# Kernel tuning notes

Hardware: AMD Instinct MI355X
Metric: run time of the kernel (lower is better)

Reference implementation:

```python
import jax, jax.numpy as jnp
import numpy as np

E = 1152          # embed_dim (Qwen3-VL vision hidden_size)
H = 16            # num_heads
D = E // H        # head_dim = 72
SEG = 8           # number of frames / attention segments
HW = 32           # each frame is 32x32 patches -> seg_len = 1024
L = HW * HW
S = SEG * L       # total tokens = 8192


def _make_rotary(S):
    # VisionRotaryEmbedding(dim=head_dim//2): inv_freq over arange(0, 36, 2)/36 -> 18 freqs
    half = D // 2  # 36
    inv_freq = 1.0 / (10000.0 ** (jnp.arange(0, half, 2, dtype=jnp.float32) / half))  # (18,)
    # 2D (h,w) position ids within each 32x32 frame, tiled across frames
    hpos = jnp.tile(jnp.repeat(jnp.arange(HW, dtype=jnp.float32), HW), SEG)  # (S,)
    wpos = jnp.tile(jnp.tile(jnp.arange(HW, dtype=jnp.float32), HW), SEG)    # (S,)
    fh = hpos[:, None] * inv_freq[None, :]   # (S, 18)
    fw = wpos[:, None] * inv_freq[None, :]   # (S, 18)
    freqs = jnp.concatenate([fh, fw], axis=-1)       # (S, 36)
    emb = jnp.concatenate([freqs, freqs], axis=-1)   # (S, 72) = head_dim
    return jnp.cos(emb), jnp.sin(emb)


def setup_inputs() -> dict:
    key = jax.random.key(0)
    k = jax.random.split(key, 6)
    std = 1.0 / np.sqrt(E)
    cos, sin = _make_rotary(S)
    return {
        "x": jax.random.normal(k[0], (S, E), jnp.float32),
        "cos": cos,
        "sin": sin,
        "qkv_w": jax.random.normal(k[1], (3 * E, E), jnp.float32) * std,
        "qkv_b": jax.random.normal(k[2], (3 * E,), jnp.float32) * 0.02,
        "proj_w": jax.random.normal(k[3], (E, E), jnp.float32) * std,
        "proj_b": jax.random.normal(k[4], (E,), jnp.float32) * 0.02,
        "cu_seqlens": jnp.arange(SEG + 1, dtype=jnp.int32) * L,
    }


def _rope(t, cos, sin):
    # t: (S, H, D); cos/sin: (S, D) broadcast over heads (matches cos.unsqueeze(1))
    half = t.shape[-1] // 2
    t1, t2 = t[..., :half], t[..., half:]
    rot = jnp.concatenate([-t2, t1], axis=-1)
    return t * cos[:, None, :] + rot * sin[:, None, :]


def reference(x, cos, sin, qkv_w, qkv_b, proj_w, proj_b, cu_seqlens):
    S_, E_ = x.shape
    qkv = x @ qkv_w.T + qkv_b                     # (S, 3E)
    q, k, v = jnp.split(qkv, 3, axis=-1)
    q = _rope(q.reshape(S_, H, D), cos, sin)
    k = _rope(k.reshape(S_, H, D), cos, sin)
    v = v.reshape(S_, H, D)
    # Equal-length segments (one per frame): block-diagonal attention via reshape,
    # honoring cu_seqlens structure without materializing an (S, S) mask.
    nseg = cu_seqlens.shape[0] - 1
    Lseg = S_ // nseg
    qs = q.reshape(nseg, Lseg, H, D)
    ks = k.reshape(nseg, Lseg, H, D)
    vs = v.reshape(nseg, Lseg, H, D)
    scale = 1.0 / np.sqrt(D)
    logits = jnp.einsum('gqhd,gkhd->ghqk', qs, ks) * scale   # (nseg, H, L, L)
    attn = jax.nn.softmax(logits, axis=-1)
    out = jnp.einsum('ghqk,gkhd->gqhd', attn, vs).reshape(S_, E_)
    return out @ proj_w.T + proj_b
```

## Files before the change

### kernel.cpp

```cpp
#include <hip/hip_runtime.h>
#include <hip/hip_bf16.h>
#include <stdint.h>

#define SEGN 8
#define LSEG 1024
#define SS   8192
#define EE   1152
#define HH   16
#define DD   72
#define DP   96
#define E3   3456
#define E3P  3584

typedef __attribute__((ext_vector_type(8))) __bf16 bf16x8;
typedef __attribute__((ext_vector_type(4))) float  f32x4;

__device__ __forceinline__ short f2b(float x) {
  __hip_bfloat16 h = __float2bfloat16(x);
  return __builtin_bit_cast(short, h);
}
__device__ __forceinline__ float b2f(short x) {
  return __bfloat162float(__builtin_bit_cast(__hip_bfloat16, x));
}
__device__ __forceinline__ void gload16(const void* g, void* l) {
  __builtin_amdgcn_global_load_lds(
      (const __attribute__((address_space(1))) unsigned int*)g,
      (__attribute__((address_space(3))) unsigned int*)l, 16, 0, 0);
}

#define BAR() __builtin_amdgcn_s_barrier()
#define LGKM0() do { asm volatile("s_waitcnt lgkmcnt(0)" ::: "memory"); \
                     __builtin_amdgcn_sched_barrier(0); } while (0)

__global__ void k_cvt(const float* __restrict__ in, short* __restrict__ out, int n4) {
  int i = blockIdx.x * blockDim.x + threadIdx.x;
  int stride = gridDim.x * blockDim.x;
  for (; i < n4; i += stride) {
    float4 v = reinterpret_cast<const float4*>(in)[i];
    short4 o;
    o.x = f2b(v.x); o.y = f2b(v.y); o.z = f2b(v.z); o.w = f2b(v.w);
    reinterpret_cast<short4*>(out)[i] = o;
  }
}

__global__ __launch_bounds__(512, 2) void k_gemm256(
    const short* __restrict__ A, const short* __restrict__ B,
    const float* __restrict__ bias, short* __restrict__ C,
    int M, int K, int Nreal)
{
  __shared__ __align__(16) short As[3][256 * 32];
  __shared__ __align__(16) short Bs[3][256 * 32];
  const int t = threadIdx.x;
  const int lane = t & 63, wave = t >> 6;
  const int r16 = lane & 15, kg = lane >> 4;
  const int wm = wave >> 2, wn = wave & 3;
  const int m0 = blockIdx.x * 256, n0 = blockIdx.y * 256;
  const int NT = K >> 5;

  const int D0 = t * 16, D1 = (t + 512) * 16;
  const int L0 = D0 ^ (((D0 >> 7) & 3) << 4);
  const int L1 = D1 ^ (((D1 >> 7) & 3) << 4);
  const int sr0 = L0 >> 6, sc0 = (L0 & 63) >> 1;
  const int sr1 = L1 >> 6, sc1 = (L1 & 63) >> 1;
  const short* pA0 = A + (size_t)(m0 + sr0) * K + sc0;
  const short* pA1 = A + (size_t)(m0 + sr1) * K + sc1;
  const short* pB0 = B + (size_t)(n0 + sr0) * K + sc0;
  const short* pB1 = B + (size_t)(n0 + sr1) * K + sc1;

  const int xorv = ((r16 >> 1) & 3) << 4;
  const int abase = (wm * 128 + r16) * 64 + ((kg * 16) ^ xorv);
  const int bbase = (wn * 64 + r16) * 64 + ((kg * 16) ^ xorv);

  f32x4 acc[8][4] = {};

  gload16(pA0, (char*)As[0] + D0); gload16(pA1, (char*)As[0] + D1);
  gload16(pB0, (char*)Bs[0] + D0); gload16(pB1, (char*)Bs[0] + D1);
  gload16(pA0 + 32, (char*)As[1] + D0); gload16(pA1 + 32, (char*)As[1] + D1);
  gload16(pB0 + 32, (char*)Bs[1] + D0); gload16(pB1 + 32, (char*)Bs[1] + D1);
  asm volatile("s_waitcnt vmcnt(4)" ::: "memory");
  BAR();

  int cur = 0;
  for (int kt = 0; kt < NT; ++kt) {
    int nb = cur + 2; if (nb >= 3) nb -= 3;
    const char* bufA = (const char*)As[cur];
    const char* bufB = (const char*)Bs[cur];
    const bool pf = (kt + 2 < NT);
    const int koff = (kt + 2) * 32;

    bf16x8 a_[4], b_[4];
#pragma unroll
    for (int m = 0; m < 4; ++m)
      a_[m] = *(const bf16x8*)(bufA + abase + m * 1024);
#pragma unroll
    for (int n = 0; n < 4; ++n)
      b_[n] = *(const bf16x8*)(bufB + bbase + n * 1024);
    if (pf) {
      gload16(pA0 + koff, (char*)As[nb] + D0);
      gload16(pA1 + koff, (char*)As[nb] + D1);
    }
    BAR();
    LGKM0();
    __builtin_amdgcn_s_setprio(1);
#pragma unroll
    for (int m = 0; m < 4; ++m)
#pragma unroll
      for (int n = 0; n < 4; ++n)
        acc[m][n] = __builtin_amdgcn_mfma_f32_16x16x32_bf16(a_[m], b_[n], acc[m][n], 0, 0, 0);
    __builtin_amdgcn_s_setprio(0);
    BAR();

    bf16x8 a2_[4];
#pragma unroll
    for (int m = 0; m < 4; ++m)
      a2_[m] = *(const bf16x8*)(bufA + abase + (m + 4) * 1024);
    if (pf) {
      gload16(pB0 + koff, (char*)Bs[nb] + D0);
      gload16(pB1 + koff, (char*)Bs[nb] + D1);
    }
    BAR();
    LGKM0();
    __builtin_amdgcn_s_setprio(1);
#pragma unroll
    for (int m = 0; m < 4; ++m)
#pragma unroll
      for (int n = 0; n < 4; ++n)
        acc[m + 4][n] = __builtin_amdgcn_mfma_f32_16x16x32_bf16(a2_[m], b_[n], acc[m + 4][n], 0, 0, 0);
    __builtin_amdgcn_s_setprio(0);
    if (pf) { asm volatile("s_waitcnt vmcnt(4)" ::: "memory"); }
    else    { asm volatile("s_waitcnt vmcnt(0)" ::: "memory"); }
    BAR();

    cur = cur + 1; if (cur >= 3) cur = 0;
  }

#pragma unroll
  for (int n = 0; n < 4; ++n) {
    int col = n0 + wn * 64 + n * 16 + r16;
    if (col < Nreal) {
      float bv = bias[col];
#pragma unroll
      for (int m = 0; m < 8; ++m)
#pragma unroll
        for (int r = 0; r < 4; ++r) {
          int row = m0 + wm * 128 + m * 16 + kg * 4 + r;
          C[(size_t)row * Nreal + col] = f2b(acc[m][n][r] + bv);
        }
    }
  }
}

__global__ __launch_bounds__(256) void k_gemm_bt_f32(
    const short* __restrict__ A, const short* __restrict__ B,
    const float* __restrict__ bias, float* __restrict__ Cout,
    int M, int N, int K)
{
  __shared__ __align__(16) short As[128 * 64];
  __shared__ __align__(16) short Bs[128 * 64];
  const int t = threadIdx.x;
  const int lane = t & 63, wave = t >> 6;
  const int r16 = lane & 15, kg = lane >> 4;
  const int m0 = blockIdx.x * 128, n0 = blockIdx.y * 128;
  const int wr = (wave >> 1) * 64, wc = (wave & 1) * 64;

  f32x4 acc[4][4] = {};

  for (int k0 = 0; k0 < K; k0 += 64) {
    __syncthreads();
#pragma unroll
    for (int i = 0; i < 4; ++i) {
      int c0 = wave * 64 + i * 256;
      int c = c0 + lane;
      int row = c >> 3, col = (c & 7) * 8;
      gload16(A + (m0 + row) * K + k0 + col, (char*)As + c0 * 16);
      gload16(B + (n0 + row) * K + k0 + col, (char*)Bs + c0 * 16);
    }
    __syncthreads();
#pragma unroll
    for (int kk = 0; kk < 2; ++kk) {
      bf16x8 a[4], b[4];
#pragma unroll
      for (int m = 0; m < 4; ++m)
        a[m] = *(const bf16x8*)&As[(wr + m * 16 + r16) * 64 + kk * 32 + kg * 8];
#pragma unroll
      for (int n = 0; n < 4; ++n)
        b[n] = *(const bf16x8*)&Bs[(wc + n * 16 + r16) * 64 + kk * 32 + kg * 8];
#pragma unroll
      for (int m = 0; m < 4; ++m)
#pragma unroll
        for (int n = 0; n < 4; ++n)
          acc[m][n] = __builtin_amdgcn_mfma_f32_16x16x32_bf16(a[m], b[n], acc[m][n], 0, 0, 0);
    }
  }

#pragma unroll
  for (int n = 0; n < 4; ++n) {
    int col = n0 + wc + n * 16 + r16;
    float bv = bias[col];
#pragma unroll
    for (int m = 0; m < 4; ++m) {
#pragma unroll
      for (int r = 0; r < 4; ++r) {
        int row = m0 + wr + m * 16 + kg * 4 + r;
        Cout[row * N + col] = acc[m][n][r] + bv;
      }
    }
  }
}

__global__ __launch_bounds__(256) void k_rope(
    const short* __restrict__ qkv, const float* __restrict__ cosb, const float* __restrict__ sinb,
    short* __restrict__ Qg, short* __restrict__ Kg, short* __restrict__ Vg)
{
  __shared__ short vt[72][64];
  const int b = blockIdx.x;
  const int seg = b >> 8, head = (b >> 4) & 15, pb = b & 15;
  const int pos0 = pb * 64;
  const int t = threadIdx.x;
  const int sh = seg * 16 + head;
  const float qscale = 0.17002540410995343f;

#pragma unroll
  for (int i = 0; i < 24; ++i) {
    int e = t + i * 256;
    int p = e / 96, d = e % 96;
    int s = seg * 1024 + pos0 + p;
    int ob = (sh * 1024 + pos0 + p) * 96 + d;
    short qo = 0, ko = 0;
    if (d < 72) {
      int base = s * E3 + head * 72;
      float c = cosb[s * 72 + d], sn = sinb[s * 72 + d];
      int d2 = d < 36 ? d + 36 : d - 36;
      float sgn = d < 36 ? -1.f : 1.f;
      float q1 = b2f(qkv[base + d]),        q2 = b2f(qkv[base + d2]);
      float k1 = b2f(qkv[base + 1152 + d]), k2 = b2f(qkv[base + 1152 + d2]);
      qo = f2b((q1 * c + sgn * q2 * sn) * qscale);
      ko = f2b(k1 * c + sgn * k2 * sn);
    }
    Qg[ob] = qo;
    Kg[ob] = ko;
  }
  for (int i = 0; i < 18; ++i) {
    int e = t + i * 256;
    int p = e / 72, d = e % 72;
    int s = seg * 1024 + pos0 + p;
    vt[d][p] = qkv[s * E3 + 2304 + head * 72 + d];
  }
  __syncthreads();
#pragma unroll
  for (int i = 0; i < 24; ++i) {
    int e = t + i * 256;
    int d = e >> 6, p = e & 63;
    short v;
    if (d < 72)       v = vt[d][p];
    else if (d == 72) v = (short)0x3F80;
    else              v = 0;
    Vg[(sh * 96 + d) * 1024 + pos0 + p] = v;
  }
}

#define KS_STRIDE 104
#define VT_STRIDE 72
#define PW_STRIDE 72
__global__ __launch_bounds__(256) void k_attn(
    const short* __restrict__ Qg, const short* __restrict__ Kg, const short* __restrict__ Vg,
    short* __restrict__ Og)
{
  __shared__ __align__(16) short Ks[64 * KS_STRIDE];
  __shared__ __align__(16) short VT[80 * VT_STRIDE];
  __shared__ __align__(16) short Pw[4][16 * PW_STRIDE];
  const int p_ = blockIdx.x;
  const int xcd = p_ & 7, rest = p_ >> 3;
  const int qb = rest & 15, shi = rest >> 4;
  const int sh = xcd * 16 + shi;
  const int seg = sh >> 4, head = sh & 15;
  const int t = threadIdx.x, lane = t & 63, wave = t >> 6;
  const int r16 = lane & 15, kg = lane >> 4;

  bf16x8 qf[3];
  {
    int row = qb * 64 + wave * 16 + r16;
    const short* qp = Qg + (sh * 1024 + row) * 96 + kg * 8;
    qf[0] = *(const bf16x8*)(qp);
    qf[1] = *(const bf16x8*)(qp + 32);
    qf[2] = *(const bf16x8*)(qp + 64);
  }
  float M_run = -1e30f;
  f32x4 acc[5] = {};

  for (int kv0 = 0; kv0 < 1024; kv0 += 64) {
    __syncthreads();
#pragma unroll
    for (int i = 0; i < 4; ++i) {
      int c0 = wave * 64 + i * 256;
      int c = c0 + lane;
      if (c < 832) {
        int row = c / 13, col8 = c % 13;
        int col = (col8 == 12) ? 0 : col8 * 8;
        gload16(Kg + (sh * 1024 + kv0 + row) * 96 + col, (char*)Ks + c0 * 16);
      }
    }
#pragma unroll
    for (int i = 0; i < 4; ++i) {
      int c0 = wave * 64 + i * 256;
      int c = c0 + lane;
      if (c < 720) {
        int d = c / 9, col8 = c % 9;
        int col = (col8 == 8) ? 0 : col8 * 8;
        gload16(Vg + (sh * 96 + d) * 1024 + kv0 + col, (char*)VT + c0 * 16);
      }
    }
    __syncthreads();

    f32x4 sacc[4] = {};
#pragma unroll
    for (int n = 0; n < 4; ++n) {
#pragma unroll
      for (int kk = 0; kk < 3; ++kk) {
        bf16x8 kb = *(const bf16x8*)&Ks[(n * 16 + r16) * KS_STRIDE + kk * 32 + kg * 8];
        sacc[n] = __builtin_amdgcn_mfma_f32_16x16x32_bf16(qf[kk], kb, sacc[n], 0, 0, 0);
      }
    }

    float tm = sacc[0][0];
#pragma unroll
    for (int n = 0; n < 4; ++n)
#pragma unroll
      for (int r = 0; r < 4; ++r)
        tm = fmaxf(tm, sacc[n][r]);
#pragma unroll
    for (int i = 1; i < 64; i <<= 1)
      tm = fmaxf(tm, __shfl_xor(tm, i));

    if (tm > M_run + 11.0f) {
      float corr = exp2f(M_run - tm);
#pragma unroll
      for (int n2 = 0; n2 < 5; ++n2)
#pragma unroll
        for (int r = 0; r < 4; ++r)
          acc[n2][r] *= corr;
      M_run = tm;
    }

    short* pw = &Pw[wave][0];
#pragma unroll
    for (int n = 0; n < 4; ++n)
#pragma unroll
      for (int r = 0; r < 4; ++r)
        pw[(kg * 4 + r) * PW_STRIDE + n * 16 + r16] = f2b(exp2f(sacc[n][r] - M_run));

#pragma unroll
    for (int kk = 0; kk < 2; ++kk) {
      bf16x8 pf = *(const bf16x8*)&pw[r16 * PW_STRIDE + kk * 32 + kg * 8];
#pragma unroll
      for (int n2 = 0; n2 < 5; ++n2) {
        bf16x8 vf = *(const bf16x8*)&VT[(n2 * 16 + r16) * VT_STRIDE + kk * 32 + kg * 8];
        acc[n2] = __builtin_amdgcn_mfma_f32_16x16x32_bf16(pf, vf, acc[n2], 0, 0, 0);
      }
    }
  }

#pragma unroll
  for (int r = 0; r < 4; ++r) {
    float l = __shfl(acc[4][r], (kg << 4) + 8);
    float inv = 1.f / l;
    int row = seg * 1024 + qb * 64 + wave * 16 + kg * 4 + r;
#pragma unroll
    for (int n2 = 0; n2 < 5; ++n2) {
      int col = n2 * 16 + r16;
      if (col < 72)
        Og[row * 1152 + head * 72 + col] = f2b(acc[n2][r] * inv);
    }
  }
}

extern "C" void kernel_launch(void* const* d_in, const int* in_sizes, int n_in,
                              void* d_out, int out_size, void* d_ws, size_t ws_size,
                              hipStream_t stream) {
  (void)in_sizes; (void)n_in; (void)out_size; (void)ws_size;
  const float* x      = (const float*)d_in[0];
  const float* cosb   = (const float*)d_in[1];
  const float* sinb   = (const float*)d_in[2];
  const float* qkv_w  = (const float*)d_in[3];
  const float* qkv_b  = (const float*)d_in[4];
  const float* proj_w = (const float*)d_in[5];
  const float* proj_b = (const float*)d_in[6];

  char* ws = (char*)d_ws;
  size_t o = 0;
  short* xb  = (short*)(ws + o); o += (size_t)SS * EE * 2;
  short* qwb = (short*)(ws + o); o += (size_t)E3P * EE * 2;
  short* pwb = (short*)(ws + o); o += (size_t)EE * EE * 2;
  short* qkv = (short*)(ws + o); o += (size_t)SS * E3 * 2;
  short* Qg  = (short*)(ws + o); o += (size_t)SEGN * HH * LSEG * DP * 2;
  short* Kg  = (short*)(ws + o); o += (size_t)SEGN * HH * LSEG * DP * 2;
  short* Vg  = (short*)(ws + o); o += (size_t)SEGN * HH * DP * LSEG * 2;
  short* og  = xb;

  k_cvt<<<2048, 256, 0, stream>>>(x, xb, SS * EE / 4);
  k_cvt<<<1024, 256, 0, stream>>>(qkv_w, qwb, E3 * EE / 4);
  k_cvt<<<512, 256, 0, stream>>>(proj_w, pwb, EE * EE / 4);

  dim3 g1(SS / 256, E3P / 256);
  k_gemm256<<<g1, 512, 0, stream>>>(xb, qwb, qkv_b, qkv, SS, EE, E3);

  k_rope<<<SEGN * HH * 16, 256, 0, stream>>>(qkv, cosb, sinb, Qg, Kg, Vg);

  k_attn<<<SEGN * HH * 16, 256, 0, stream>>>(Qg, Kg, Vg, og);

  dim3 g2(SS / 128, EE / 128);
  k_gemm_bt_f32<<<g2, 256, 0, stream>>>(og, pwb, proj_b, (float*)d_out, SS, EE, EE);
}
```

Baseline: 299.0 us.

## Rewrite attention kernel with 32x32 MFMA tiles and register-resident P

Switches the flash-attention kernel from 16x16x32 to 32x32x16 bf16 MFMA. Each wave now handles 32 query rows, so a block covers 128 queries and the grid is halved. It computes S^T so the probabilities stay in registers and are rearranged with cross-lane shuffles instead of being staged through shared memory. Load offsets are precomputed, per-row running max is used with a lazy rescale threshold, and launch bounds request 3 blocks per CU. The larger accumulators raise register pressure, and halving the block count may reduce occupancy or load balance.

```diff
diff --git a/kernel.cpp b/kernel.cpp
--- a/kernel.cpp
+++ b/kernel.cpp
@@ -12,8 +12,10 @@
 #define E3   3456
 #define E3P  3584
 
-typedef __attribute__((ext_vector_type(8))) __bf16 bf16x8;
-typedef __attribute__((ext_vector_type(4))) float  f32x4;
+typedef __attribute__((ext_vector_type(8)))  __bf16 bf16x8;
+typedef __attribute__((ext_vector_type(4)))  float  f32x4;
+typedef __attribute__((ext_vector_type(16))) float  f32x16;
+typedef __attribute__((ext_vector_type(4)))  unsigned int u32x4;
 
 __device__ __forceinline__ short f2b(float x) {
   __hip_bfloat16 h = __float2bfloat16(x);
@@ -21,6 +23,10 @@
 }
 __device__ __forceinline__ float b2f(short x) {
   return __bfloat162float(__builtin_bit_cast(__hip_bfloat16, x));
+}
+__device__ __forceinline__ unsigned int pk2(float x, float y) {
+  return (unsigned int)(unsigned short)f2b(x) |
+         ((unsigned int)(unsigned short)f2b(y) << 16);
 }
 __device__ __forceinline__ void gload16(const void* g, void* l) {
   __builtin_amdgcn_global_load_lds(
@@ -259,118 +265,129 @@
   }
 }
 
-#define KS_STRIDE 104
-#define VT_STRIDE 72
-#define PW_STRIDE 72
-__global__ __launch_bounds__(256) void k_attn(
+#define KSS 104
+#define VTS 72
+__global__ __launch_bounds__(256, 3) void k_attn(
     const short* __restrict__ Qg, const short* __restrict__ Kg, const short* __restrict__ Vg,
     short* __restrict__ Og)
 {
-  __shared__ __align__(16) short Ks[64 * KS_STRIDE];
-  __shared__ __align__(16) short VT[80 * VT_STRIDE];
-  __shared__ __align__(16) short Pw[4][16 * PW_STRIDE];
+  __shared__ __align__(16) short Ks[64 * KSS];
+  __shared__ __align__(16) short VT[96 * VTS];
   const int p_ = blockIdx.x;
   const int xcd = p_ & 7, rest = p_ >> 3;
-  const int qb = rest & 15, shi = rest >> 4;
+  const int qb = rest & 7, shi = rest >> 3;
   const int sh = xcd * 16 + shi;
   const int seg = sh >> 4, head = sh & 15;
   const int t = threadIdx.x, lane = t & 63, wave = t >> 6;
-  const int r16 = lane & 15, kg = lane >> 4;
-
-  bf16x8 qf[3];
+  const int l31 = lane & 31, hi = lane >> 5;
+  const int q0 = qb * 128 + wave * 32;
+
+  bf16x8 qf[6];
   {
-    int row = qb * 64 + wave * 16 + r16;
-    const short* qp = Qg + (sh * 1024 + row) * 96 + kg * 8;
-    qf[0] = *(const bf16x8*)(qp);
-    qf[1] = *(const bf16x8*)(qp + 32);
-    qf[2] = *(const bf16x8*)(qp + 64);
-  }
-  float M_run = -1e30f;
-  f32x4 acc[5] = {};
-
-  for (int kv0 = 0; kv0 < 1024; kv0 += 64) {
+    const short* qp = Qg + ((size_t)(sh * 1024 + q0 + l31)) * 96 + hi * 8;
+#pragma unroll
+    for (int dm = 0; dm < 6; ++dm) qf[dm] = *(const bf16x8*)(qp + dm * 16);
+  }
+
+  const short* kbase = Kg + (size_t)sh * 1024 * 96;
+  const short* vbase = Vg + (size_t)sh * 96 * 1024;
+  int koff[4], voff[4];
+#pragma unroll
+  for (int i = 0; i < 4; ++i) {
+    int c = t + i * 256;
+    int kr = c / 13, kc8 = c - kr * 13;
+    koff[i] = kr * 96 + ((kc8 == 12) ? 0 : kc8 * 8);
+    int vr = c / 9, vc8 = c - vr * 9;
+    voff[i] = vr * 1024 + ((vc8 == 8) ? 0 : vc8 * 8);
+  }
+
+  f32x16 acc0 = {}, acc1 = {}, acc2 = {};
+  float Mrun = -1e30f;
+
+  for (int kt = 0; kt < 16; ++kt) {
     __syncthreads();
-#pragma unroll
-    for (int i = 0; i < 4; ++i) {
-      int c0 = wave * 64 + i * 256;
-      int c = c0 + lane;
-      if (c < 832) {
-        int row = c / 13, col8 = c % 13;
-        int col = (col8 == 12) ? 0 : col8 * 8;
-        gload16(Kg + (sh * 1024 + kv0 + row) * 96 + col, (char*)Ks + c0 * 16);
+    {
+      const short* kp = kbase + kt * 64 * 96;
+      const short* vp = vbase + kt * 64;
+#pragma unroll
+      for (int i = 0; i < 3; ++i) {
+        gload16(kp + koff[i], (char*)Ks + (t + i * 256) * 16);
+        gload16(vp + voff[i], (char*)VT + (t + i * 256) * 16);
       }
-    }
-#pragma unroll
-    for (int i = 0; i < 4; ++i) {
-      int c0 = wave * 64 + i * 256;
-      int c = c0 + lane;
-      if (c < 720) {
-        int d = c / 9, col8 = c % 9;
-        int col = (col8 == 8) ? 0 : col8 * 8;
-        gload16(Vg + (sh * 96 + d) * 1024 + kv0 + col, (char*)VT + c0 * 16);
+      if (t < 64) gload16(kp + koff[3], (char*)Ks + (t + 768) * 16);
+      if (t < 96) gload16(vp + voff[3], (char*)VT + (t + 768) * 16);
+    }
+    __syncthreads();
+
+    f32x16 s0 = {}, s1 = {};
+#pragma unroll
+    for (int dm = 0; dm < 6; ++dm) {
+      bf16x8 kf0 = *(const bf16x8*)&Ks[l31 * KSS + dm * 16 + hi * 8];
+      bf16x8 kf1 = *(const bf16x8*)&Ks[(32 + l31) * KSS + dm * 16 + hi * 8];
+      s0 = __builtin_amdgcn_mfma_f32_32x32x16_bf16(kf0, qf[dm], s0, 0, 0, 0);
+      s1 = __builtin_amdgcn_mfma_f32_32x32x16_bf16(kf1, qf[dm], s1, 0, 0, 0);
+    }
+
+    float pmax = s0[0];
+#pragma unroll
+    for (int r = 1; r < 16; ++r) pmax = fmaxf(pmax, s0[r]);
+#pragma unroll
+    for (int r = 0; r < 16; ++r) pmax = fmaxf(pmax, s1[r]);
+    pmax = fmaxf(pmax, __shfl_xor(pmax, 32));
+
+    if (__any(pmax > Mrun + 8.0f)) {
+      float mn = fmaxf(Mrun, pmax);
+      float corr = exp2f(Mrun - mn);
+      Mrun = mn;
+#pragma unroll
+      for (int r = 0; r < 16; ++r) {
+        int qr = (r & 3) + 8 * (r >> 2) + 4 * hi;
+        float cr = __shfl(corr, qr);
+        acc0[r] *= cr; acc1[r] *= cr; acc2[r] *= cr;
       }
     }
-    __syncthreads();
-
-    f32x4 sacc[4] = {};
-#pragma unroll
-    for (int n = 0; n < 4; ++n) {
-#pragma unroll
-      for (int kk = 0; kk < 3; ++kk) {
-        bf16x8 kb = *(const bf16x8*)&Ks[(n * 16 + r16) * KS_STRIDE + kk * 32 + kg * 8];
-        sacc[n] = __builtin_amdgcn_mfma_f32_16x16x32_bf16(qf[kk], kb, sacc[n], 0, 0, 0);
+
+    unsigned int pk0[8], pk1[8];
+#pragma unroll
+    for (int b = 0; b < 4; ++b)
+#pragma unroll
+      for (int i = 0; i < 2; ++i) {
+        pk0[b * 2 + i] = pk2(exp2f(s0[b * 4 + 2 * i] - Mrun), exp2f(s0[b * 4 + 2 * i + 1] - Mrun));
+        pk1[b * 2 + i] = pk2(exp2f(s1[b * 4 + 2 * i] - Mrun), exp2f(s1[b * 4 + 2 * i + 1] - Mrun));
       }
-    }
-
-    float tm = sacc[0][0];
-#pragma unroll
-    for (int n = 0; n < 4; ++n)
-#pragma unroll
-      for (int r = 0; r < 4; ++r)
-        tm = fmaxf(tm, sacc[n][r]);
-#pragma unroll
-    for (int i = 1; i < 64; i <<= 1)
-      tm = fmaxf(tm, __shfl_xor(tm, i));
-
-    if (tm > M_run + 11.0f) {
-      float corr = exp2f(M_run - tm);
-#pragma unroll
-      for (int n2 = 0; n2 < 5; ++n2)
-#pragma unroll
-        for (int r = 0; r < 4; ++r)
-          acc[n2][r] *= corr;
-      M_run = tm;
-    }
-
-    short* pw = &Pw[wave][0];
-#pragma unroll
-    for (int n = 0; n < 4; ++n)
-#pragma unroll
-      for (int r = 0; r < 4; ++r)
-        pw[(kg * 4 + r) * PW_STRIDE + n * 16 + r16] = f2b(exp2f(sacc[n][r] - M_run));
-
-#pragma unroll
-    for (int kk = 0; kk < 2; ++kk) {
-      bf16x8 pf = *(const bf16x8*)&pw[r16 * PW_STRIDE + kk * 32 + kg * 8];
-#pragma unroll
-      for (int n2 = 0; n2 < 5; ++n2) {
-        bf16x8 vf = *(const bf16x8*)&VT[(n2 * 16 + r16) * VT_STRIDE + kk * 32 + kg * 8];
-        acc[n2] = __builtin_amdgcn_mfma_f32_16x16x32_bf16(pf, vf, acc[n2], 0, 0, 0);
-      }
-    }
-  }
-
-#pragma unroll
-  for (int r = 0; r < 4; ++r) {
-    float l = __shfl(acc[4][r], (kg << 4) + 8);
-    float inv = 1.f / l;
-    int row = seg * 1024 + qb * 64 + wave * 16 + kg * 4 + r;
-#pragma unroll
-    for (int n2 = 0; n2 < 5; ++n2) {
-      int col = n2 * 16 + r16;
-      if (col < 72)
-        Og[row * 1152 + head * 72 + col] = f2b(acc[n2][r] * inv);
-    }
+
+#pragma unroll
+    for (int ks = 0; ks < 4; ++ks) {
+      const int k1 = ks & 1;
+      unsigned int A0, A1, B0, B1;
+      if (ks < 2) { A0 = pk0[4 * k1]; A1 = pk0[4 * k1 + 1]; B0 = pk0[4 * k1 + 2]; B1 = pk0[4 * k1 + 3]; }
+      else        { A0 = pk1[4 * k1]; A1 = pk1[4 * k1 + 1]; B0 = pk1[4 * k1 + 2]; B1 = pk1[4 * k1 + 3]; }
+      unsigned int SA0 = __shfl_xor((int)A0, 32), SA1 = __shfl_xor((int)A1, 32);
+      unsigned int SB0 = __shfl_xor((int)B0, 32), SB1 = __shfl_xor((int)B1, 32);
+      u32x4 wv;
+      wv.x = hi ? SB0 : A0;
+      wv.y = hi ? SB1 : A1;
+      wv.z = hi ? B0 : SA0;
+      wv.w = hi ? B1 : SA1;
+      bf16x8 af = __builtin_bit_cast(bf16x8, wv);
+      bf16x8 vf0 = *(const bf16x8*)&VT[l31 * VTS + ks * 16 + hi * 8];
+      bf16x8 vf1 = *(const bf16x8*)&VT[(32 + l31) * VTS + ks * 16 + hi * 8];
+      bf16x8 vf2 = *(const bf16x8*)&VT[(64 + l31) * VTS + ks * 16 + hi * 8];
+      acc0 = __builtin_amdgcn_mfma_f32_32x32x16_bf16(af, vf0, acc0, 0, 0, 0);
+      acc1 = __builtin_amdgcn_mfma_f32_32x32x16_bf16(af, vf1, acc1, 0, 0, 0);
+      acc2 = __builtin_amdgcn_mfma_f32_32x32x16_bf16(af, vf2, acc2, 0, 0, 0);
+    }
+  }
+
+#pragma unroll
+  for (int r = 0; r < 16; ++r) {
+    float l = __shfl(acc2[r], (lane & 32) | 8);
+    float inv = 1.0f / l;
+    int q = q0 + (r & 3) + 8 * (r >> 2) + 4 * hi;
+    size_t base = (size_t)(seg * 1024 + q) * 1152 + head * 72;
+    Og[base + l31]      = f2b(acc0[r] * inv);
+    Og[base + 32 + l31] = f2b(acc1[r] * inv);
+    if (l31 < 8) Og[base + 64 + l31] = f2b(acc2[r] * inv);
   }
 }
 
@@ -406,7 +423,7 @@
 
   k_rope<<<SEGN * HH * 16, 256, 0, stream>>>(qkv, cosb, sinb, Qg, Kg, Vg);
 
-  k_attn<<<SEGN * HH * 16, 256, 0, stream>>>(Qg, Kg, Vg, og);
+  k_attn<<<SEGN * HH * 8, 256, 0, stream>>>(Qg, Kg, Vg, og);
 
   dim3 g2(SS / 128, EE / 128);
   k_gemm_bt_f32<<<g2, 256, 0, stream>>>(og, pwb, proj_b, (float*)d_out, SS, EE, EE);
```

Measured after the change: 284.9 us. 4.7% less time.
